# Kernel tuning notes

Hardware: AMD Instinct MI355X
Metric: run time of the kernel (lower is better)

The kernel has to match this reference:

```python
import jax, jax.numpy as jnp
import numpy as np

WS = 21                      # window_size
K = 2 * WS + 1               # window_length = 43
SIGMA_COLOR = 1.0 / (0.1 * 0.1 * 2.0)   # 50.0
SIGMA_SPACE = 1.0 / (7.0 * 7.0 * 2.0)
LP = 0.8
C1 = 20.0
C2 = 10.0


def edge_response(im):
    """EdgeResponse (not given in snippet): Sobel gradient magnitude summed over channels -> (B,H,W)."""
    B, C, H, W = im.shape
    p = jnp.pad(im, ((0, 0), (0, 0), (1, 1), (1, 1)), mode='reflect')
    kx = jnp.array([[-1, 0, 1], [-2, 0, 2], [-1, 0, 1]], jnp.float32)
    ky = kx.T
    x = p.reshape(B * C, 1, H + 2, W + 2)
    gx = jax.lax.conv_general_dilated(x, kx[None, None], (1, 1), 'VALID').reshape(B, C, H, W)
    gy = jax.lax.conv_general_dilated(x, ky[None, None], (1, 1), 'VALID').reshape(B, C, H, W)
    return jnp.sqrt(gx * gx + gy * gy).sum(1)


def safe_pow(d, p):
    # d >= 0; forward identical to d**p (0**0.8 == 0), but avoids inf grad at d==0
    dsafe = jnp.where(d > 0, d, 1.0)
    return jnp.where(d > 0, dsafe ** p, 0.0)


def setup_inputs() -> dict:
    key = jax.random.key(0)
    k1, k2 = jax.random.split(key)
    original_images = jax.random.normal(k1, (2, 3, 128, 128), dtype=jnp.float32)
    smooth_images = jax.random.normal(k2, (2, 3, 128, 128), dtype=jnp.float32)
    return {"original_images": original_images, "smooth_images": smooth_images}


def reference(original_images, smooth_images):
    B, C, H, W = original_images.shape
    eo = edge_response(original_images)
    es = edge_response(smooth_images)
    m_large = ((eo < C1) & (es - eo > C2)).astype(jnp.float32)[:, None]  # (B,1,H,W)
    m_small = 1.0 - m_large

    pad = lambda im: jnp.pad(im, ((0, 0), (0, 0), (WS, WS), (WS, WS)), mode='reflect')
    sp = pad(smooth_images)
    op = pad(original_images)

    offs = jnp.array([(x, y) for x in range(-WS, WS + 1) for y in range(-WS, WS + 1)], jnp.int32)

    @jax.checkpoint
    def step(acc, off):
        x, y = off[0], off[1]
        s_sh = jax.lax.dynamic_slice(sp, (0, 0, WS + x, WS + y), (B, C, H, W))
        o_sh = jax.lax.dynamic_slice(op, (0, 0, WS + x, WS + y), (B, C, H, W))
        d = jnp.abs(smooth_images - s_sh)                       # |Ti - Tj|
        wr = jnp.exp(-SIGMA_COLOR * ((original_images - o_sh) ** 2).sum(1))[:, None]  # (B,1,H,W)
        xf = x.astype(jnp.float32)
        yf = y.astype(jnp.float32)
        ws_w = jnp.exp(-SIGMA_SPACE * (xf * xf + yf * yf))       # scalar spatial weight
        term = m_large * ws_w * (d * d) + m_small * wr * safe_pow(d, LP)
        return acc + term.sum(), None

    total, _ = jax.lax.scan(step, jnp.float32(0.0), offs)
    return total / (H * W * B)
```

## Files before the change

### kernel.cpp

```cpp
#include <hip/hip_runtime.h>
#include <math.h>

#define WS 21
#define KWIN 43
#define H 128
#define W 128
#define B 2
#define C 3
#define HW (H * W)
#define CHW (C * H * W)
#define NPIX (B * H * W)
#define SIGMA_SPACE (1.0f / 98.0f)
#define NSPLIT 8
#define SQ_THR_FP16 0.17f
#define NEG_SC_LOG2E 72.1347520445f
#define SG 17.509290f
#define WSLOTS 108

typedef _Float16 h2_t __attribute__((ext_vector_type(2)));

#define LDS_COMPILER_FENCE() asm volatile("" ::: "memory")

__device__ __forceinline__ int reflect_idx(int t, int n) {
    if (t < 0) t = -t;
    if (t > n - 1) t = 2 * (n - 1) - t;
    return t;
}

__global__ __launch_bounds__(384)
void prep_kernel(const float* __restrict__ orig,
                 const float* __restrict__ smooth,
                 float* __restrict__ Gh, float* __restrict__ Qh,
                 float* __restrict__ mask, float* __restrict__ out) {
    __shared__ float row[170], rsq[170], wt[KWIN];
    const int bid = blockIdx.x;
    const int h   = bid & 127;
    const int bc  = bid >> 7;
    const int t   = threadIdx.x;
    if (bid == 0 && t == 0) out[0] = 0.f;
    if (t < KWIN) { int k = t - WS; wt[t] = __expf(-SIGMA_SPACE * (float)(k * k)); }
    const float* src = smooth + bc * HW + h * W;
    if (t < 170) {
        float v = src[reflect_idx(t - WS, W)];
        row[t] = v; rsq[t] = v * v;
    }
    __syncthreads();
    if (t < 256) {
        const int w = t & 127;
        const float* buf = (t < 128) ? row : rsq;
        float acc = 0.f;
#pragma unroll
        for (int y = 0; y < KWIN; ++y) acc = fmaf(wt[y], buf[w + y], acc);
        ((t < 128) ? Gh : Qh)[bid * W + w] = acc;
    } else if (bc == 0 || bc == 3) {
        const int b = bc / 3;
        const int w = t - 256;
        const float* ob = orig   + b * CHW;
        const float* sb = smooth + b * CHW;
        int hm = reflect_idx(h - 1, H), hp = reflect_idx(h + 1, H);
        int wm = reflect_idx(w - 1, W), wp = reflect_idx(w + 1, W);
        float eo = 0.f, es = 0.f;
#pragma unroll
        for (int c = 0; c < C; ++c) {
            const float* po = ob + c * HW;
            const float* ps = sb + c * HW;
            {
                float a00 = po[hm * W + wm], a01 = po[hm * W + w], a02 = po[hm * W + wp];
                float a10 = po[h  * W + wm],                        a12 = po[h  * W + wp];
                float a20 = po[hp * W + wm], a21 = po[hp * W + w], a22 = po[hp * W + wp];
                float gx = (a02 - a00) + 2.f * (a12 - a10) + (a22 - a20);
                float gy = (a20 - a00) + 2.f * (a21 - a01) + (a22 - a02);
                eo += sqrtf(gx * gx + gy * gy);
            }
            {
                float a00 = ps[hm * W + wm], a01 = ps[hm * W + w], a02 = ps[hm * W + wp];
                float a10 = ps[h  * W + wm],                        a12 = ps[h  * W + wp];
                float a20 = ps[hp * W + wm], a21 = ps[hp * W + w], a22 = ps[hp * W + wp];
                float gx = (a02 - a00) + 2.f * (a12 - a10) + (a22 - a20);
                float gy = (a20 - a00) + 2.f * (a21 - a01) + (a22 - a02);
                es += sqrtf(gx * gx + gy * gy);
            }
        }
        float m = ((eo < 20.0f) && ((es - eo) > 10.0f)) ? 1.0f : 0.0f;
        mask[(b << 14) + (h << 7) + w] = m;
    }
}

__global__ __launch_bounds__(256)
void screen_kernel(const float* __restrict__ orig,
                   const float* __restrict__ smooth,
                   const float* __restrict__ Gh, const float* __restrict__ Qh,
                   const float* __restrict__ mask,
                   float* __restrict__ out) {
    __shared__ uint2 oA[4 * WSLOTS];
    __shared__ float red[4];

    const int t    = threadIdx.x;
    const int wave = t >> 6;
    const int lane = t & 63;
    const int gw   = blockIdx.x * 4 + wave;
    const int split = gw & 7;
    const int half  = (gw >> 3) & 1;
    const int h     = (gw >> 4) & 127;
    const int b     = gw >> 11;
    const int w0    = half * 64;
    const int w     = w0 + lane;
    const int wb    = wave * WSLOTS;

    const float* ob  = orig   + b * CHW;
    const float* sb  = smooth + b * CHW;
    const float* GhB = Gh + b * 3 * HW;
    const float* QhB = Qh + b * 3 * HW;

    const int pix = (b << 14) + (h << 7) + w;
    const float m = mask[pix];
    const float thr_l = (m == 0.0f) ? SQ_THR_FP16 : -1.0f;

    float o0c, o1c, o2c, s0c, s1c, s2c;
    {
        int hw = h * W + w;
        o0c = ob[hw]; o1c = ob[HW + hw]; o2c = ob[2 * HW + hw];
        s0c = sb[hw]; s1c = sb[HW + hw]; s2c = sb[2 * HW + hw];
    }
    const h2_t c01h = { (_Float16)o0c, (_Float16)o1c };
    const h2_t c2xh = { (_Float16)o2c, (_Float16)0.f };

    const float n0 = s0c * s0c * SG, n1 = s1c * s1c * SG, n2 = s2c * s2c * SG;
    const float tc0 = -2.f * s0c, tc1 = -2.f * s1c, tc2 = -2.f * s2c;

    const int  sc1  = reflect_idx(w0 - WS + lane, W);
    const bool has2 = (lane < 42);
    const int  sc2  = reflect_idx(w0 + 43 + lane, W);

    float accAL = 0.f, accS = 0.f;

    float a0, a1, a2, b0 = 0.f, b1 = 0.f, b2 = 0.f;
    {
        const int rr0 = reflect_idx(h + split - WS, H);
        const float* prow = ob + rr0 * W;
        a0 = prow[sc1]; a1 = prow[HW + sc1]; a2 = prow[2 * HW + sc1];
        if (has2) { b0 = prow[sc2]; b1 = prow[HW + sc2]; b2 = prow[2 * HW + sc2]; }
    }

    for (int xi = split; xi < KWIN; xi += NSPLIT) {
        const int x  = xi - WS;
        const int rr = reflect_idx(h + x, H);

        LDS_COMPILER_FENCE();
        {
            h2_t v01 = { (_Float16)a0, (_Float16)a1 };
            h2_t v2x = { (_Float16)a2, (_Float16)0.f };
            oA[wb + lane] = make_uint2(__builtin_bit_cast(unsigned, v01),
                                       __builtin_bit_cast(unsigned, v2x));
            if (has2) {
                h2_t u01 = { (_Float16)b0, (_Float16)b1 };
                h2_t u2x = { (_Float16)b2, (_Float16)0.f };
                oA[wb + 64 + lane] = make_uint2(__builtin_bit_cast(unsigned, u01),
                                                __builtin_bit_cast(unsigned, u2x));
            }
        }
        LDS_COMPILER_FENCE();

        const int xin = xi + NSPLIT;
        if (xin < KWIN) {
            const int rrn = reflect_idx(h + xin - WS, H);
            const float* prow = ob + rrn * W;
            a0 = prow[sc1]; a1 = prow[HW + sc1]; a2 = prow[2 * HW + sc1];
            if (has2) { b0 = prow[sc2]; b1 = prow[HW + sc2]; b2 = prow[2 * HW + sc2]; }
        }

        {
            const int ga = rr * W + w;
            float G0 = GhB[ga], G1 = GhB[HW + ga], G2 = GhB[2 * HW + ga];
            float Q0 = QhB[ga], Q1 = QhB[HW + ga], Q2 = QhB[2 * HW + ga];
            float xf = (float)x;
            float wtx = __expf(-SIGMA_SPACE * xf * xf);
            float gsum = (n0 + fmaf(tc0, G0, Q0))
                       + (n1 + fmaf(tc1, G1, Q1))
                       + (n2 + fmaf(tc2, G2, Q2));
            accAL = fmaf(wtx, gsum, accAL);
        }

        unsigned mA = 0u, mB_ = 0u;
#pragma unroll
        for (int yi = 0; yi < KWIN; ++yi) {
            uint2 vv = oA[wb + lane + yi];
            h2_t p01 = __builtin_bit_cast(h2_t, vv.x);
            h2_t p2x = __builtin_bit_cast(h2_t, vv.y);
            h2_t d01 = c01h - p01;
            h2_t d2x = c2xh - p2x;
            float sq = __builtin_amdgcn_fdot2(d01, d01,
                        __builtin_amdgcn_fdot2(d2x, d2x, 0.f, false), false);
            unsigned bit = (sq < thr_l) ? 1u : 0u;
            if (yi < 21) mA  = (mA  << 1) | bit;
            else         mB_ = (mB_ << 1) | bit;
        }
        if (xi == WS) mB_ &= ~(1u << 21);

        while (mA | mB_) {
            int yi;
            if (mA) { int p = __builtin_ctz(mA); mA &= mA - 1; yi = 20 - p; }
            else    { int p = __builtin_ctz(mB_); mB_ &= mB_ - 1; yi = 42 - p; }
            int ww = reflect_idx(w + yi - WS, W);
            int a = rr * W + ww;
            float on0 = ob[a], on1 = ob[HW + a], on2 = ob[2 * HW + a];
            float sn0 = sb[a], sn1 = sb[HW + a], sn2 = sb[2 * HW + a];
            float g0 = o0c - on0, g1 = o1c - on1, g2 = o2c - on2;
            float sq = fmaf(g0, g0, fmaf(g1, g1, g2 * g2));
            float tt = -NEG_SC_LOG2E * sq;
            float d0 = fabsf(s0c - sn0), d1 = fabsf(s1c - sn1), d2 = fabsf(s2c - sn2);
            accS += __builtin_amdgcn_exp2f(fmaf(0.8f, __builtin_amdgcn_logf(d0), tt))
                  + __builtin_amdgcn_exp2f(fmaf(0.8f, __builtin_amdgcn_logf(d1), tt))
                  + __builtin_amdgcn_exp2f(fmaf(0.8f, __builtin_amdgcn_logf(d2), tt));
        }
        LDS_COMPILER_FENCE();
    }

    float r = m * accAL + accS;
#pragma unroll
    for (int off = 32; off > 0; off >>= 1) r += __shfl_down(r, off, 64);
    if (lane == 0) red[wave] = r;
    __syncthreads();
    if (t == 0) atomicAdd(out, (red[0] + red[1] + red[2] + red[3]) * (1.0f / (float)NPIX));
}

extern "C" void kernel_launch(void* const* d_in, const int* in_sizes, int n_in,
                              void* d_out, int out_size, void* d_ws, size_t ws_size,
                              hipStream_t stream) {
    const float* orig   = (const float*)d_in[0];
    const float* smooth = (const float*)d_in[1];
    float* out = (float*)d_out;

    float* Gh  = (float*)d_ws;
    float* Qh  = Gh + B * C * HW;
    float* msk = Qh + B * C * HW;

    prep_kernel<<<B * C * H, 384, 0, stream>>>(orig, smooth, Gh, Qh, msk, out);
    screen_kernel<<<(B * H * 2 * NSPLIT) / 4, 256, 0, stream>>>(orig, smooth, Gh, Qh, msk, out);
}
```

Baseline: 85.36 us.

## Process two adjacent pixels per lane sharing one LDS window row

Each wave now covers a full 128-wide row, with every lane handling two adjacent pixels instead of one. Window row values are stored in LDS with an even/odd interleaved layout, so each LDS read feeds the screening of both pixels. The row-offset split grows from 8 to 16, which keeps the total wave count unchanged. This cuts per-pixel LDS loads and global loads (G/Q/mask now read as float2), at the cost of more registers and serialized sparse loops for two pixels per lane.

Measured after the change: 89.47 us. 4.8% more time.

```diff
diff --git a/kernel.cpp b/kernel.cpp
--- a/kernel.cpp
+++ b/kernel.cpp
@@ -11,11 +11,11 @@
 #define CHW (C * H * W)
 #define NPIX (B * H * W)
 #define SIGMA_SPACE (1.0f / 98.0f)
-#define NSPLIT 8
+#define NSPLIT 16
 #define SQ_THR_FP16 0.17f
 #define NEG_SC_LOG2E 72.1347520445f
 #define SG 17.509290f
-#define WSLOTS 108
+#define WSLOTS 172
 
 typedef _Float16 h2_t __attribute__((ext_vector_type(2)));
 
@@ -99,12 +99,10 @@
     const int wave = t >> 6;
     const int lane = t & 63;
     const int gw   = blockIdx.x * 4 + wave;
-    const int split = gw & 7;
-    const int half  = (gw >> 3) & 1;
+    const int split = gw & 15;
     const int h     = (gw >> 4) & 127;
     const int b     = gw >> 11;
-    const int w0    = half * 64;
-    const int w     = w0 + lane;
+    const int w0    = lane * 2;
     const int wb    = wave * WSLOTS;
 
     const float* ob  = orig   + b * CHW;
@@ -112,35 +110,48 @@
     const float* GhB = Gh + b * 3 * HW;
     const float* QhB = Qh + b * 3 * HW;
 
-    const int pix = (b << 14) + (h << 7) + w;
-    const float m = mask[pix];
-    const float thr_l = (m == 0.0f) ? SQ_THR_FP16 : -1.0f;
-
-    float o0c, o1c, o2c, s0c, s1c, s2c;
-    {
-        int hw = h * W + w;
-        o0c = ob[hw]; o1c = ob[HW + hw]; o2c = ob[2 * HW + hw];
-        s0c = sb[hw]; s1c = sb[HW + hw]; s2c = sb[2 * HW + hw];
-    }
-    const h2_t c01h = { (_Float16)o0c, (_Float16)o1c };
-    const h2_t c2xh = { (_Float16)o2c, (_Float16)0.f };
-
-    const float n0 = s0c * s0c * SG, n1 = s1c * s1c * SG, n2 = s2c * s2c * SG;
-    const float tc0 = -2.f * s0c, tc1 = -2.f * s1c, tc2 = -2.f * s2c;
-
-    const int  sc1  = reflect_idx(w0 - WS + lane, W);
+    float2 mm = ((const float2*)(mask + (b << 14) + (h << 7)))[lane];
+    const float thr0 = (mm.x == 0.0f) ? SQ_THR_FP16 : -1.0f;
+    const float thr1 = (mm.y == 0.0f) ? SQ_THR_FP16 : -1.0f;
+
+    float2 o0 = ((const float2*)(ob + h * W))[lane];
+    float2 o1 = ((const float2*)(ob + HW + h * W))[lane];
+    float2 o2 = ((const float2*)(ob + 2 * HW + h * W))[lane];
+    float2 s0 = ((const float2*)(sb + h * W))[lane];
+    float2 s1 = ((const float2*)(sb + HW + h * W))[lane];
+    float2 s2 = ((const float2*)(sb + 2 * HW + h * W))[lane];
+
+    const h2_t c01h0 = { (_Float16)o0.x, (_Float16)o1.x };
+    const h2_t c2xh0 = { (_Float16)o2.x, (_Float16)0.f };
+    const h2_t c01h1 = { (_Float16)o0.y, (_Float16)o1.y };
+    const h2_t c2xh1 = { (_Float16)o2.y, (_Float16)0.f };
+
+    const float n00 = o0.x * 0.f + s0.x * s0.x * SG, n01 = s1.x * s1.x * SG, n02 = s2.x * s2.x * SG;
+    const float n10 = s0.y * s0.y * SG, n11 = s1.y * s1.y * SG, n12 = s2.y * s2.y * SG;
+    const float tc00 = -2.f * s0.x, tc01 = -2.f * s1.x, tc02 = -2.f * s2.x;
+    const float tc10 = -2.f * s0.y, tc11 = -2.f * s1.y, tc12 = -2.f * s2.y;
+
+    const int  e0 = lane,      i0 = (e0 & 1) * 86 + (e0 >> 1);
+    const int  e1 = lane + 64, i1 = (e1 & 1) * 86 + (e1 >> 1);
     const bool has2 = (lane < 42);
-    const int  sc2  = reflect_idx(w0 + 43 + lane, W);
-
-    float accAL = 0.f, accS = 0.f;
-
-    float a0, a1, a2, b0 = 0.f, b1 = 0.f, b2 = 0.f;
+    const int  e2 = lane + 128, i2 = (e2 & 1) * 86 + (e2 >> 1);
+    const int  sA_ = reflect_idx(e0 - WS, W);
+    const int  sB_ = reflect_idx(e1 - WS, W);
+    const int  sC_ = reflect_idx(e2 - WS, W);
+
+    float accAL0 = 0.f, accAL1 = 0.f, accS = 0.f;
+
+    float A0, A1, A2, B0, B1, B2, C0 = 0.f, C1 = 0.f, C2_ = 0.f;
     {
         const int rr0 = reflect_idx(h + split - WS, H);
         const float* prow = ob + rr0 * W;
-        a0 = prow[sc1]; a1 = prow[HW + sc1]; a2 = prow[2 * HW + sc1];
-        if (has2) { b0 = prow[sc2]; b1 = prow[HW + sc2]; b2 = prow[2 * HW + sc2]; }
-    }
+        A0 = prow[sA_]; A1 = prow[HW + sA_]; A2 = prow[2 * HW + sA_];
+        B0 = prow[sB_]; B1 = prow[HW + sB_]; B2 = prow[2 * HW + sB_];
+        if (has2) { C0 = prow[sC_]; C1 = prow[HW + sC_]; C2_ = prow[2 * HW + sC_]; }
+    }
+
+    const uint2* pE = oA + wb + lane;
+    const uint2* pO = oA + wb + 86 + lane;
 
     for (int xi = split; xi < KWIN; xi += NSPLIT) {
         const int x  = xi - WS;
@@ -148,15 +159,19 @@
 
         LDS_COMPILER_FENCE();
         {
-            h2_t v01 = { (_Float16)a0, (_Float16)a1 };
-            h2_t v2x = { (_Float16)a2, (_Float16)0.f };
-            oA[wb + lane] = make_uint2(__builtin_bit_cast(unsigned, v01),
-                                       __builtin_bit_cast(unsigned, v2x));
+            h2_t v01 = { (_Float16)A0, (_Float16)A1 };
+            h2_t v2x = { (_Float16)A2, (_Float16)0.f };
+            oA[wb + i0] = make_uint2(__builtin_bit_cast(unsigned, v01),
+                                     __builtin_bit_cast(unsigned, v2x));
+            h2_t u01 = { (_Float16)B0, (_Float16)B1 };
+            h2_t u2x = { (_Float16)B2, (_Float16)0.f };
+            oA[wb + i1] = make_uint2(__builtin_bit_cast(unsigned, u01),
+                                     __builtin_bit_cast(unsigned, u2x));
             if (has2) {
-                h2_t u01 = { (_Float16)b0, (_Float16)b1 };
-                h2_t u2x = { (_Float16)b2, (_Float16)0.f };
-                oA[wb + 64 + lane] = make_uint2(__builtin_bit_cast(unsigned, u01),
-                                                __builtin_bit_cast(unsigned, u2x));
+                h2_t y01 = { (_Float16)C0, (_Float16)C1 };
+                h2_t y2x = { (_Float16)C2_, (_Float16)0.f };
+                oA[wb + i2] = make_uint2(__builtin_bit_cast(unsigned, y01),
+                                         __builtin_bit_cast(unsigned, y2x));
             }
         }
         LDS_COMPILER_FENCE();
@@ -165,58 +180,94 @@
         if (xin < KWIN) {
             const int rrn = reflect_idx(h + xin - WS, H);
             const float* prow = ob + rrn * W;
-            a0 = prow[sc1]; a1 = prow[HW + sc1]; a2 = prow[2 * HW + sc1];
-            if (has2) { b0 = prow[sc2]; b1 = prow[HW + sc2]; b2 = prow[2 * HW + sc2]; }
+            A0 = prow[sA_]; A1 = prow[HW + sA_]; A2 = prow[2 * HW + sA_];
+            B0 = prow[sB_]; B1 = prow[HW + sB_]; B2 = prow[2 * HW + sB_];
+            if (has2) { C0 = prow[sC_]; C1 = prow[HW + sC_]; C2_ = prow[2 * HW + sC_]; }
         }
 
         {
-            const int ga = rr * W + w;
-            float G0 = GhB[ga], G1 = GhB[HW + ga], G2 = GhB[2 * HW + ga];
-            float Q0 = QhB[ga], Q1 = QhB[HW + ga], Q2 = QhB[2 * HW + ga];
+            float2 G0 = ((const float2*)(GhB + rr * W))[lane];
+            float2 G1 = ((const float2*)(GhB + HW + rr * W))[lane];
+            float2 G2 = ((const float2*)(GhB + 2 * HW + rr * W))[lane];
+            float2 Q0 = ((const float2*)(QhB + rr * W))[lane];
+            float2 Q1 = ((const float2*)(QhB + HW + rr * W))[lane];
+            float2 Q2 = ((const float2*)(QhB + 2 * HW + rr * W))[lane];
             float xf = (float)x;
             float wtx = __expf(-SIGMA_SPACE * xf * xf);
-            float gsum = (n0 + fmaf(tc0, G0, Q0))
-                       + (n1 + fmaf(tc1, G1, Q1))
-                       + (n2 + fmaf(tc2, G2, Q2));
-            accAL = fmaf(wtx, gsum, accAL);
-        }
-
-        unsigned mA = 0u, mB_ = 0u;
-#pragma unroll
-        for (int yi = 0; yi < KWIN; ++yi) {
-            uint2 vv = oA[wb + lane + yi];
+            float g0 = (n00 + fmaf(tc00, G0.x, Q0.x))
+                     + (n01 + fmaf(tc01, G1.x, Q1.x))
+                     + (n02 + fmaf(tc02, G2.x, Q2.x));
+            float g1 = (n10 + fmaf(tc10, G0.y, Q0.y))
+                     + (n11 + fmaf(tc11, G1.y, Q1.y))
+                     + (n12 + fmaf(tc12, G2.y, Q2.y));
+            accAL0 = fmaf(wtx, g0, accAL0);
+            accAL1 = fmaf(wtx, g1, accAL1);
+        }
+
+        unsigned mA0 = 0u, mB0 = 0u, mA1 = 0u, mB1 = 0u;
+#pragma unroll
+        for (int i = 0; i < 44; ++i) {
+            uint2 vv = (i & 1) ? pO[i >> 1] : pE[i >> 1];
             h2_t p01 = __builtin_bit_cast(h2_t, vv.x);
             h2_t p2x = __builtin_bit_cast(h2_t, vv.y);
-            h2_t d01 = c01h - p01;
-            h2_t d2x = c2xh - p2x;
-            float sq = __builtin_amdgcn_fdot2(d01, d01,
-                        __builtin_amdgcn_fdot2(d2x, d2x, 0.f, false), false);
-            unsigned bit = (sq < thr_l) ? 1u : 0u;
-            if (yi < 21) mA  = (mA  << 1) | bit;
-            else         mB_ = (mB_ << 1) | bit;
-        }
-        if (xi == WS) mB_ &= ~(1u << 21);
-
-        while (mA | mB_) {
+            if (i <= 42) {
+                h2_t d01 = c01h0 - p01;
+                h2_t d2x = c2xh0 - p2x;
+                float sq = __builtin_amdgcn_fdot2(d01, d01,
+                            __builtin_amdgcn_fdot2(d2x, d2x, 0.f, false), false);
+                unsigned bit = (sq < thr0) ? 1u : 0u;
+                if (i < 21) mA0 |= bit << (20 - i);
+                else        mB0 |= bit << (42 - i);
+            }
+            if (i >= 1) {
+                const int yi = i - 1;
+                h2_t d01 = c01h1 - p01;
+                h2_t d2x = c2xh1 - p2x;
+                float sq = __builtin_amdgcn_fdot2(d01, d01,
+                            __builtin_amdgcn_fdot2(d2x, d2x, 0.f, false), false);
+                unsigned bit = (sq < thr1) ? 1u : 0u;
+                if (yi < 21) mA1 |= bit << (20 - yi);
+                else         mB1 |= bit << (42 - yi);
+            }
+        }
+        if (xi == WS) { mB0 &= ~(1u << 21); mB1 &= ~(1u << 21); }
+
+        while (mA0 | mB0) {
             int yi;
-            if (mA) { int p = __builtin_ctz(mA); mA &= mA - 1; yi = 20 - p; }
-            else    { int p = __builtin_ctz(mB_); mB_ &= mB_ - 1; yi = 42 - p; }
-            int ww = reflect_idx(w + yi - WS, W);
+            if (mA0) { int p = __builtin_ctz(mA0); mA0 &= mA0 - 1; yi = 20 - p; }
+            else     { int p = __builtin_ctz(mB0); mB0 &= mB0 - 1; yi = 42 - p; }
+            int ww = reflect_idx(w0 + yi - WS, W);
             int a = rr * W + ww;
             float on0 = ob[a], on1 = ob[HW + a], on2 = ob[2 * HW + a];
             float sn0 = sb[a], sn1 = sb[HW + a], sn2 = sb[2 * HW + a];
-            float g0 = o0c - on0, g1 = o1c - on1, g2 = o2c - on2;
+            float g0 = o0.x - on0, g1 = o1.x - on1, g2 = o2.x - on2;
             float sq = fmaf(g0, g0, fmaf(g1, g1, g2 * g2));
             float tt = -NEG_SC_LOG2E * sq;
-            float d0 = fabsf(s0c - sn0), d1 = fabsf(s1c - sn1), d2 = fabsf(s2c - sn2);
+            float d0 = fabsf(s0.x - sn0), d1 = fabsf(s1.x - sn1), d2 = fabsf(s2.x - sn2);
             accS += __builtin_amdgcn_exp2f(fmaf(0.8f, __builtin_amdgcn_logf(d0), tt))
                   + __builtin_amdgcn_exp2f(fmaf(0.8f, __builtin_amdgcn_logf(d1), tt))
                   + __builtin_amdgcn_exp2f(fmaf(0.8f, __builtin_amdgcn_logf(d2), tt));
         }
+        while (mA1 | mB1) {
+            int yi;
+            if (mA1) { int p = __builtin_ctz(mA1); mA1 &= mA1 - 1; yi = 20 - p; }
+            else     { int p = __builtin_ctz(mB1); mB1 &= mB1 - 1; yi = 42 - p; }
+            int ww = reflect_idx(w0 + 1 + yi - WS, W);
+            int a = rr * W + ww;
+            float on0 = ob[a], on1 = ob[HW + a], on2 = ob[2 * HW + a];
+            float sn0 = sb[a], sn1 = sb[HW + a], sn2 = sb[2 * HW + a];
+            float g0 = o0.y - on0, g1 = o1.y - on1, g2 = o2.y - on2;
+            float sq = fmaf(g0, g0, fmaf(g1, g1, g2 * g2));
+            float tt = -NEG_SC_LOG2E * sq;
+            float d0 = fabsf(s0.y - sn0), d1 = fabsf(s1.y - sn1), d2 = fabsf(s2.y - sn2);
+            accS += __builtin_amdgcn_exp2f(fmaf(0.8f, __builtin_amdgcn_logf(d0), tt))
+                  + __builtin_amdgcn_exp2f(fmaf(0.8f, __builtin_amdgcn_logf(d1), tt))
+                  + __builtin_amdgcn_exp2f(fmaf(0.8f, __builtin_amdgcn_logf(d2), tt));
+        }
         LDS_COMPILER_FENCE();
     }
 
-    float r = m * accAL + accS;
+    float r = mm.x * accAL0 + mm.y * accAL1 + accS;
 #pragma unroll
     for (int off = 32; off > 0; off >>= 1) r += __shfl_down(r, off, 64);
     if (lane == 0) red[wave] = r;
@@ -236,5 +287,5 @@
     float* msk = Qh + B * C * HW;
 
     prep_kernel<<<B * C * H, 384, 0, stream>>>(orig, smooth, Gh, Qh, msk, out);
-    screen_kernel<<<(B * H * 2 * NSPLIT) / 4, 256, 0, stream>>>(orig, smooth, Gh, Qh, msk, out);
-}
+    screen_kernel<<<(B * H * NSPLIT) / 4, 256, 0, stream>>>(orig, smooth, Gh, Qh, msk, out);
+}
```
